# Kernel tuning notes

Hardware: AMD Instinct MI355X
Metric: run time of the kernel (lower is better)

The kernel has to match this reference:

```python
import jax, jax.numpy as jnp
import numpy as np
from jax import lax
from itertools import product

KS = 3          # kernel_size
PAD = 1         # padding
N = KS ** 3     # 27 sample points per voxel


def _conv3d_3x3(x, w, b):
    # x: [b,c,D,H,W], w: [O,c,3,3,3]
    out = lax.conv_general_dilated(x, w, (1, 1, 1), [(PAD, PAD)] * 3,
                                   dimension_numbers=('NCDHW', 'OIDHW', 'NCDHW'))
    return out + b[None, :, None, None, None]


def setup_inputs() -> dict:
    key = jax.random.key(0)
    k1, k2, k3, k4 = jax.random.split(key, 4)
    B, C, D, OUTC = 2, 32, 24, 64
    x = jax.random.normal(k1, (B, C, D, D, D), jnp.float32)
    p_w = jax.random.normal(k2, (3 * N, C, KS, KS, KS), jnp.float32) * 0.02
    p_b = jax.random.normal(k3, (3 * N,), jnp.float32) * 0.02
    conv_w = jax.random.normal(k4, (OUTC, C * N), jnp.float32) / np.sqrt(C * N)
    return {"x": x, "p_w": p_w, "p_b": p_b, "conv_w": conv_w}


def reference(x, p_w, p_b, conv_w):
    b, c, h, w, d = x.shape
    # offset prediction: [b, 3N, h, w, d]
    offset = _conv3d_3x3(x, p_w, p_b)

    # p_n: kernel-relative offsets, p_0: base grid (shifted by +1 for padding)
    r = np.arange(-(KS - 1) // 2, (KS - 1) // 2 + 1)
    gx, gy, gz = np.meshgrid(r, r, r, indexing='ij')
    p_n = jnp.asarray(np.concatenate([gx.ravel(), gy.ravel(), gz.ravel()])
                      .reshape(1, 3 * N, 1, 1, 1), jnp.float32)
    ox, oy, oz = np.meshgrid(np.arange(1, h + 1), np.arange(1, w + 1),
                             np.arange(1, d + 1), indexing='ij')
    def rep(a):
        return np.broadcast_to(a.reshape(1, 1, h, w, d), (1, N, h, w, d))
    p_0 = jnp.asarray(np.concatenate([rep(ox), rep(oy), rep(oz)], axis=1), jnp.float32)

    p = p_0 + p_n + offset                      # [b, 3N, h, w, d]
    p = jnp.transpose(p, (0, 2, 3, 4, 1))        # [b, h, w, d, 3N]

    xp = jnp.pad(x, ((0, 0), (0, 0), (PAD, PAD), (PAD, PAD), (PAD, PAD)))
    sizes = (xp.shape[2], xp.shape[3], xp.shape[4])
    ps = [p[..., :N], p[..., N:2 * N], p[..., 2 * N:]]

    qs, ql, pm = [], [], []
    for ax in range(3):
        s = sizes[ax]
        f = jnp.floor(ps[ax])
        qs.append(jnp.clip(f, 0, s - 1).astype(jnp.int32))
        ql.append(jnp.clip(f + 1, 0, s - 1).astype(jnp.int32))
        # out-of-range mask: snap p to its floor (matches torch detach + floor_p)
        m = lax.stop_gradient(((ps[ax] < PAD) | (ps[ax] > s - 1 - PAD)).astype(ps[ax].dtype))
        pa = ps[ax] * (1 - m) + f * m
        pm.append(jnp.clip(pa, 0, s - 1))

    def gather(xb, qi, qj, qk):
        return xb[:, qi, qj, qk]  # [c, h, w, d, N]

    acc = jnp.zeros((b, c, h, w, d, N), x.dtype)
    for cx, cy, cz in product((0, 1), repeat=3):   # 8 trilinear corners
        bits = (cx, cy, cz)
        q = [qs[a] if bits[a] == 0 else ql[a] for a in range(3)]
        g = jnp.ones_like(pm[0])
        for a in range(3):
            diff = q[a].astype(pm[a].dtype) - pm[a]
            g = g * ((1 + diff) if bits[a] == 0 else (1 - diff))
        xq = jax.vmap(gather)(xp, q[0], q[1], q[2])  # [b, c, h, w, d, N]
        acc = acc + g[:, None] * xq

    # [b,c,h,w,d,N] -> [b, c*N, h, w, d] (c-major, N-minor, as in torch view)
    x_off = jnp.transpose(acc, (0, 1, 5, 2, 3, 4)).reshape(b, c * N, h, w, d)
    out = jnp.einsum('oi,bidhw->bodhw', conv_w, x_off)
    p_out = jnp.concatenate(pm, axis=-1)
    return out, p_out
```

## Files before the change

kernel.cpp:

```cpp
#include <hip/hip_runtime.h>

#define CC 32
#define DIM 24
#define SP (DIM*DIM*DIM)
#define NPTS 27
#define M3 81
#define OUTC 64
#define BATCH 2
#define CN (CC*NPTS)

#define VBB 12
#define NV (NPTS*VBB)
#define CPAD 896
#define MP 84
#define HROW 26
#define HALOF (32*3*4*HROW)

typedef __attribute__((ext_vector_type(8))) short short8;
typedef __attribute__((ext_vector_type(4))) float f32x4;

__device__ __forceinline__ unsigned short f2bf(float f) {
    unsigned u = __builtin_bit_cast(unsigned, f);
    return (unsigned short)((u + 0x7FFFu + ((u >> 16) & 1u)) >> 16);
}

__global__ __launch_bounds__(256)
void prep_w_kernel(const float* __restrict__ p_w,
                   const float* __restrict__ conv_w,
                   float* __restrict__ p_wTP,
                   unsigned short* __restrict__ conv_wbf) {
    int id = blockIdx.x * 256 + threadIdx.x;
    if (id < CN * MP) {
        int k = id / MP, m = id % MP;
        p_wTP[id] = (m < M3) ? p_w[(size_t)m * CN + k] : 0.f;
    }
    if (id < CN * OUTC) {
        int o = id / CN, kp = id % CN;
        int n = kp >> 5, c = kp & 31;
        conv_wbf[id] = f2bf(conv_w[(size_t)o * CN + c * NPTS + n]);
    }
}

__global__ __launch_bounds__(256)
void transpose_x_kernel(const float* __restrict__ x,
                        unsigned short* __restrict__ x_t) {
    __shared__ float tile[CC][65];
    int b = blockIdx.x / 216;
    int sp0 = (blockIdx.x % 216) * 64;
    const float* xb = x + (size_t)b * CC * SP;
    for (int it = threadIdx.x; it < CC * 64; it += 256) {
        int c = it >> 6, s = it & 63;
        tile[c][s] = xb[(size_t)c * SP + sp0 + s];
    }
    __syncthreads();
    unsigned short* xtb = x_t + (size_t)b * SP * CC;
    for (int it = threadIdx.x; it < CC * 64; it += 256) {
        int s = it >> 5, c = it & 31;
        xtb[(size_t)(sp0 + s) * CC + c] = f2bf(tile[c][s]);
    }
}

__global__ __launch_bounds__(512, 4)
void offset_gemm_kernel(const float* __restrict__ x,
                        const float* __restrict__ p_wTP,
                        const float* __restrict__ p_b,
                        float* __restrict__ offset) {
    __shared__ float lds[HALOF];

    int bid = blockIdx.x;
    int jp = bid % 12;
    int i  = (bid / 12) % 24;
    int b  = bid / 288;
    int j0 = jp * 2;
    int sp0 = i * 576 + j0 * 24;
    int t = threadIdx.x;

    for (int it = t; it < HALOF; it += 512) {
        int rh = it / HROW, u = it - rh * HROW;
        int c = rh / 12, r2 = rh - c * 12;
        int di = r2 >> 2, jq = r2 & 3;
        int ii = i + di - 1, jj = j0 - 1 + jq, kk = u - 1;
        bool v = ((unsigned)ii < (unsigned)DIM) && ((unsigned)jj < (unsigned)DIM) &&
                 ((unsigned)kk < (unsigned)DIM);
        lds[it] =
            v ? x[((size_t)(b * CC + c) * SP) + ii * 576 + jj * 24 + kk] : 0.f;
    }
    __syncthreads();

    int w = t >> 6, l = t & 63;
    int mt = l / 3, vt = l % 3;
    bool act = (l < 63);
    if (mt > 20) mt = 20;

    float acc[4][8], ac2[4][8];
    #pragma unroll
    for (int a = 0; a < 4; ++a)
        #pragma unroll
        for (int e = 0; e < 8; ++e) { acc[a][e] = 0.f; ac2[a][e] = 0.f; }

    const float* gw = p_wTP + (size_t)(w * 108) * MP + mt * 4;

    for (int cdij = 0; cdij < 36; ++cdij) {
        int c = 4 * w + cdij / 9;
        int dij = cdij % 9;
        int di = dij / 3, dj = dij % 3;
        const float* xrA = lds + ((c * 3 + di) * 4 + dj) * HROW + vt * 8;
        const float* xrB = xrA + HROW;

        float2 a0 = *(const float2*)(xrA);
        float2 a1 = *(const float2*)(xrA + 2);
        float2 a2 = *(const float2*)(xrA + 4);
        float2 a3 = *(const float2*)(xrA + 6);
        float2 a4 = *(const float2*)(xrA + 8);
        float xvA[10] = { a0.x, a0.y, a1.x, a1.y, a2.x, a2.y,
                          a3.x, a3.y, a4.x, a4.y };
        float2 b0 = *(const float2*)(xrB);
        float2 b1 = *(const float2*)(xrB + 2);
        float2 b2 = *(const float2*)(xrB + 4);
        float2 b3 = *(const float2*)(xrB + 6);
        float2 b4 = *(const float2*)(xrB + 8);
        float xvB[10] = { b0.x, b0.y, b1.x, b1.y, b2.x, b2.y,
                          b3.x, b3.y, b4.x, b4.y };

        const float* wr = gw + (size_t)(cdij * 3) * MP;
        #pragma unroll
        for (int dk = 0; dk < 3; ++dk) {
            float4 wv = *(const float4*)(wr + (size_t)dk * MP);
            #pragma unroll
            for (int e = 0; e < 8; ++e) {
                float xa = xvA[dk + e];
                float xb = xvB[dk + e];
                acc[0][e] += wv.x * xa;  ac2[0][e] += wv.x * xb;
                acc[1][e] += wv.y * xa;  ac2[1][e] += wv.y * xb;
                acc[2][e] += wv.z * xa;  ac2[2][e] += wv.z * xb;
                acc[3][e] += wv.w * xa;  ac2[3][e] += wv.w * xb;
            }
        }
    }
    __syncthreads();

    float* part = lds;
    #define STORE_P(W)                                                      \
        do {                                                                \
            float* dst = &part[((W) * MP + mt * 4) * 48 + vt * 8];          \
            _Pragma("unroll")                                               \
            for (int a = 0; a < 4; ++a) {                                   \
                _Pragma("unroll")                                           \
                for (int e2 = 0; e2 < 2; ++e2) {                            \
                    *(float4*)&dst[a * 48 + e2 * 4] =                       \
                        make_float4(acc[a][e2*4], acc[a][e2*4+1],           \
                                    acc[a][e2*4+2], acc[a][e2*4+3]);        \
                    *(float4*)&dst[a * 48 + 24 + e2 * 4] =                  \
                        make_float4(ac2[a][e2*4], ac2[a][e2*4+1],           \
                                    ac2[a][e2*4+2], ac2[a][e2*4+3]);        \
                }                                                           \
            }                                                               \
        } while (0)
    #define ADD_P(W)                                                       \
        do {                                                                \
            float* dst = &part[((W) * MP + mt * 4) * 48 + vt * 8];          \
            _Pragma("unroll")                                               \
            for (int a = 0; a < 4; ++a) {                                   \
                _Pragma("unroll")                                           \
                for (int e2 = 0; e2 < 2; ++e2) {                            \
                    float4 p = *(const float4*)&dst[a * 48 + e2 * 4];       \
                    p.x += acc[a][e2*4];   p.y += acc[a][e2*4+1];           \
                    p.z += acc[a][e2*4+2]; p.w += acc[a][e2*4+3];           \
                    *(float4*)&dst[a * 48 + e2 * 4] = p;                    \
                    float4 q = *(const float4*)&dst[a * 48 + 24 + e2 * 4];  \
                    q.x += ac2[a][e2*4];   q.y += ac2[a][e2*4+1];           \
                    q.z += ac2[a][e2*4+2]; q.w += ac2[a][e2*4+3];           \
                    *(float4*)&dst[a * 48 + 24 + e2 * 4] = q;               \
                }                                                           \
            }                                                               \
        } while (0)

    if (act && w < 2) STORE_P(w);
    __syncthreads();
    if (act && (w == 2 || w == 3)) ADD_P(w - 2);
    __syncthreads();
    if (act && (w == 4 || w == 5)) ADD_P(w - 4);
    __syncthreads();
    if (act && (w == 6 || w == 7)) ADD_P(w - 6);
    __syncthreads();
    #undef STORE_P
    #undef ADD_P

    for (int it = t; it < M3 * 12; it += 512) {
        int m = it / 12, vq = it % 12;
        float4 p0 = *(const float4*)&part[(m) * 48 + vq * 4];
        float4 p1 = *(const float4*)&part[(MP + m) * 48 + vq * 4];
        float bias = p_b[m];
        float4 s = make_float4(p0.x + p1.x + bias, p0.y + p1.y + bias,
                               p0.z + p1.z + bias, p0.w + p1.w + bias);
        *(float4*)&offset[((size_t)(b * M3 + m)) * SP + sp0 + vq * 4] = s;
    }
}

__global__ __launch_bounds__(256, 4)
void sample_gemm_kernel(const unsigned short* __restrict__ x_t,
                        const float* __restrict__ offset,
                        const unsigned short* __restrict__ conv_wbf,
                        float* __restrict__ out,
                        float* __restrict__ p_out) {
    __shared__ __align__(16) unsigned char region[VBB * CPAD * 2 + 8 * NV * 4];
    unsigned short* col = (unsigned short*)region;
    unsigned* s_corner = (unsigned*)(region + VBB * CPAD * 2);

    int bid = blockIdx.x;
    int r = bid & 1;
    int j = (bid >> 1) % 24;
    int i = ((bid >> 1) / 24) % 24;
    int b = bid / 1152;
    int k0 = r * VBB;
    int sp0 = i * 576 + j * 24 + k0;
    int t = threadIdx.x;

    const unsigned short* xtb = x_t + (size_t)b * SP * CC;

    for (int it = t; it < NV; it += 256) {
        int v = it % VBB, n = it / VBB;
        int sp = sp0 + v;
        int k = k0 + v;

        int pnx = n / 9 - 1, pny = (n / 3) % 3 - 1, pnz = n % 3 - 1;
        float p0a[3] = { (float)(i + 1 + pnx),
                         (float)(j + 1 + pny),
                         (float)(k + 1 + pnz) };
        int ql[3], qh[3];
        float wl[3], wh[3];
        #pragma unroll
        for (int ax = 0; ax < 3; ++ax) {
            int m = ax * NPTS + n;
            float p = p0a[ax] + offset[((size_t)(b * M3 + m)) * SP + sp];
            float f = floorf(p);
            int qlo = (int)fminf(fmaxf(f,       0.f), 25.f);
            int qhi = (int)fminf(fmaxf(f + 1.f, 0.f), 25.f);
            bool oob = (p < 1.f) || (p > 24.f);
            float pa = oob ? f : p;
            float pm = fminf(fmaxf(pa, 0.f), 25.f);
            ql[ax] = qlo; qh[ax] = qhi;
            wl[ax] = 1.f + ((float)qlo - pm);
            wh[ax] = 1.f - ((float)qhi - pm);
            p_out[((size_t)(b * SP + sp)) * M3 + m] = pm;
        }

        #pragma unroll
        for (int cr = 0; cr < 8; ++cr) {
            int ii = ((cr & 4) ? qh[0] : ql[0]) - 1;
            int jj = ((cr & 2) ? qh[1] : ql[1]) - 1;
            int kk = ((cr & 1) ? qh[2] : ql[2]) - 1;
            bool valid = ((unsigned)ii < (unsigned)DIM) &&
                         ((unsigned)jj < (unsigned)DIM) &&
                         ((unsigned)kk < (unsigned)DIM);
            float cw = ((cr & 4) ? wh[0] : wl[0]) *
                       ((cr & 2) ? wh[1] : wl[1]) *
                       ((cr & 1) ? wh[2] : wl[2]);
            unsigned idx = (unsigned)(ii * 576 + jj * 24 + kk);
            s_corner[cr * NV + it] =
                valid ? ((idx << 16) | (unsigned)f2bf(cw)) : 0u;
        }
    }
    __syncthreads();

    for (int task = t; task < NV * 4; task += 256) {
        int item = task >> 2, q = task & 3;
        int v = item % VBB, n = item / VBB;

        const unsigned short* xq = xtb + q * 8;
        float acc[8];
        #pragma unroll
        for (int e = 0; e < 8; ++e) acc[e] = 0.f;

        #pragma unroll
        for (int cr = 0; cr < 8; ++cr) {
            unsigned u = s_corner[cr * NV + item];
            float wc = __builtin_bit_cast(float, u << 16);
            const unsigned* s = (const unsigned*)(xq + (size_t)(u >> 16) * CC);
            #pragma unroll
            for (int q2 = 0; q2 < 4; ++q2) {
                unsigned uu = s[q2];
                acc[2 * q2]     += wc * __builtin_bit_cast(float, uu << 16);
                acc[2 * q2 + 1] += wc * __builtin_bit_cast(float, uu & 0xFFFF0000u);
            }
        }

        short8 pk;
        #pragma unroll
        for (int e = 0; e < 8; ++e)
            pk[e] = (short)f2bf(acc[e]);
        int sv = (v & 7) << 3;
        *(short8*)&col[v * CPAD + ((n * 32 + q * 8) ^ sv)] = pk;
    }
    __syncthreads();

    {
        int mt = t >> 6;
        int l = t & 63;
        int lr = l & 15;
        int g = l >> 4;
        int sv = (lr & 7) << 3;

        const short8* ap =
            (const short8*)(conv_wbf + ((size_t)(mt * 16 + lr)) * CN + g * 8);
        const unsigned short* bp = col + lr * CPAD;

        f32x4 acc = {0.f, 0.f, 0.f, 0.f};
        #pragma unroll 3
        for (int kb = 0; kb < CN / 32; ++kb) {
            short8 a = ap[kb * 4];
            short8 bb = *(const short8*)&bp[(kb * 32 + g * 8) ^ sv];
            acc = __builtin_amdgcn_mfma_f32_16x16x32_bf16(a, bb, acc, 0, 0, 0);
        }
        if (lr < VBB) {
            float* op = out + ((size_t)(b * OUTC + mt * 16 + g * 4)) * SP + sp0 + lr;
            #pragma unroll
            for (int rr = 0; rr < 4; ++rr)
                op[(size_t)rr * SP] = acc[rr];
        }
    }
}

extern "C" void kernel_launch(void* const* d_in, const int* in_sizes, int n_in,
                              void* d_out, int out_size, void* d_ws, size_t ws_size,
                              hipStream_t stream) {
    const float* x      = (const float*)d_in[0];
    const float* p_w    = (const float*)d_in[1];
    const float* p_b    = (const float*)d_in[2];
    const float* conv_w = (const float*)d_in[3];

    float* out_all = (float*)d_out;
    float* out_main = out_all;
    float* p_out    = out_all + (size_t)BATCH * OUTC * SP;

    float* offset          = (float*)d_ws;
    float* p_wTP           = offset + (size_t)BATCH * M3 * SP;
    unsigned short* conv_wbf = (unsigned short*)(p_wTP + (size_t)CN * MP);
    unsigned short* x_t    = conv_wbf + (size_t)CN * OUTC;

    {
        int total = CN * MP;
        prep_w_kernel<<<(total + 255) / 256, 256, 0, stream>>>(p_w, conv_w,
                                                               p_wTP, conv_wbf);
    }
    {
        int blocks = BATCH * (SP / 64);
        transpose_x_kernel<<<blocks, 256, 0, stream>>>(x, x_t);
    }
    {
        int blocks = BATCH * 24 * 12;
        offset_gemm_kernel<<<blocks, 512, 0, stream>>>(x, p_wTP, p_b, offset);
    }
    {
        int blocks = BATCH * 24 * 24 * 2;
        sample_gemm_kernel<<<blocks, 256, 0, stream>>>(x_t, offset, conv_wbf,
                                                       out_main, p_out);
    }
}
```

Baseline: 123.5 us.

## Restructure offset conv: wave-per-output-channel-slice with scalar weights, drop LDS reduction

```diff
diff --git a/kernel.cpp b/kernel.cpp
--- a/kernel.cpp
+++ b/kernel.cpp
@@ -14,7 +14,7 @@
 #define CPAD 896
 #define MP 84
 #define HROW 26
-#define HALOF (32*3*4*HROW)
+#define HALOF (CC*3*4*HROW)
 
 typedef __attribute__((ext_vector_type(8))) short short8;
 typedef __attribute__((ext_vector_type(4))) float f32x4;
@@ -60,12 +60,12 @@
     }
 }
 
-__global__ __launch_bounds__(512, 4)
+__global__ __launch_bounds__(256, 4)
 void offset_gemm_kernel(const float* __restrict__ x,
                         const float* __restrict__ p_wTP,
                         const float* __restrict__ p_b,
                         float* __restrict__ offset) {
-    __shared__ float lds[HALOF];
+    __shared__ float halo[HALOF];
 
     int bid = blockIdx.x;
     int jp = bid % 12;
@@ -75,125 +75,57 @@
     int sp0 = i * 576 + j0 * 24;
     int t = threadIdx.x;
 
-    for (int it = t; it < HALOF; it += 512) {
+    for (int it = t; it < HALOF; it += 256) {
         int rh = it / HROW, u = it - rh * HROW;
         int c = rh / 12, r2 = rh - c * 12;
         int di = r2 >> 2, jq = r2 & 3;
         int ii = i + di - 1, jj = j0 - 1 + jq, kk = u - 1;
         bool v = ((unsigned)ii < (unsigned)DIM) && ((unsigned)jj < (unsigned)DIM) &&
                  ((unsigned)kk < (unsigned)DIM);
-        lds[it] =
+        halo[it] =
             v ? x[((size_t)(b * CC + c) * SP) + ii * 576 + jj * 24 + kk] : 0.f;
     }
     __syncthreads();
 
-    int w = t >> 6, l = t & 63;
-    int mt = l / 3, vt = l % 3;
-    bool act = (l < 63);
-    if (mt > 20) mt = 20;
-
-    float acc[4][8], ac2[4][8];
+    int l = t & 63;
+    int wu = __builtin_amdgcn_readfirstlane(t >> 6);
+    bool act = (l < 48);
+    int vl = act ? l : 47;
+    int jrow = vl / 24, kv = vl - jrow * 24;
+    int lane_base = jrow * HROW + kv;
+
+    float acc[21];
     #pragma unroll
-    for (int a = 0; a < 4; ++a)
-        #pragma unroll
-        for (int e = 0; e < 8; ++e) { acc[a][e] = 0.f; ac2[a][e] = 0.f; }
-
-    const float* gw = p_wTP + (size_t)(w * 108) * MP + mt * 4;
-
-    for (int cdij = 0; cdij < 36; ++cdij) {
-        int c = 4 * w + cdij / 9;
-        int dij = cdij % 9;
-        int di = dij / 3, dj = dij % 3;
-        const float* xrA = lds + ((c * 3 + di) * 4 + dj) * HROW + vt * 8;
-        const float* xrB = xrA + HROW;
-
-        float2 a0 = *(const float2*)(xrA);
-        float2 a1 = *(const float2*)(xrA + 2);
-        float2 a2 = *(const float2*)(xrA + 4);
-        float2 a3 = *(const float2*)(xrA + 6);
-        float2 a4 = *(const float2*)(xrA + 8);
-        float xvA[10] = { a0.x, a0.y, a1.x, a1.y, a2.x, a2.y,
-                          a3.x, a3.y, a4.x, a4.y };
-        float2 b0 = *(const float2*)(xrB);
-        float2 b1 = *(const float2*)(xrB + 2);
-        float2 b2 = *(const float2*)(xrB + 4);
-        float2 b3 = *(const float2*)(xrB + 6);
-        float2 b4 = *(const float2*)(xrB + 8);
-        float xvB[10] = { b0.x, b0.y, b1.x, b1.y, b2.x, b2.y,
-                          b3.x, b3.y, b4.x, b4.y };
-
-        const float* wr = gw + (size_t)(cdij * 3) * MP;
-        #pragma unroll
-        for (int dk = 0; dk < 3; ++dk) {
-            float4 wv = *(const float4*)(wr + (size_t)dk * MP);
+    for (int mm = 0; mm < 21; ++mm) acc[mm] = 0.f;
+
+    const float* wbase = p_wTP + 21 * wu;
+
+    for (int c = 0; c < CC; ++c) {
+        const float* hb = halo + c * (3 * 4 * HROW) + lane_base;
+        const float* wc = wbase + (size_t)(c * 27) * MP;
+        #pragma unroll
+        for (int dij = 0; dij < 9; ++dij) {
+            int di = dij / 3, dj = dij % 3;
+            const float* hrow = hb + (di * 4 + dj) * HROW;
             #pragma unroll
-            for (int e = 0; e < 8; ++e) {
-                float xa = xvA[dk + e];
-                float xb = xvB[dk + e];
-                acc[0][e] += wv.x * xa;  ac2[0][e] += wv.x * xb;
-                acc[1][e] += wv.y * xa;  ac2[1][e] += wv.y * xb;
-                acc[2][e] += wv.z * xa;  ac2[2][e] += wv.z * xb;
-                acc[3][e] += wv.w * xa;  ac2[3][e] += wv.w * xb;
+            for (int dk = 0; dk < 3; ++dk) {
+                float xv = hrow[dk];
+                const float* wr = wc + (size_t)(dij * 3 + dk) * MP;
+                #pragma unroll
+                for (int mm = 0; mm < 21; ++mm)
+                    acc[mm] += wr[mm] * xv;
             }
         }
     }
-    __syncthreads();
-
-    float* part = lds;
-    #define STORE_P(W)                                                      \
-        do {                                                                \
-            float* dst = &part[((W) * MP + mt * 4) * 48 + vt * 8];          \
-            _Pragma("unroll")                                               \
-            for (int a = 0; a < 4; ++a) {                                   \
-                _Pragma("unroll")                                           \
-                for (int e2 = 0; e2 < 2; ++e2) {                            \
-                    *(float4*)&dst[a * 48 + e2 * 4] =                       \
-                        make_float4(acc[a][e2*4], acc[a][e2*4+1],           \
-                                    acc[a][e2*4+2], acc[a][e2*4+3]);        \
-                    *(float4*)&dst[a * 48 + 24 + e2 * 4] =                  \
-                        make_float4(ac2[a][e2*4], ac2[a][e2*4+1],           \
-                                    ac2[a][e2*4+2], ac2[a][e2*4+3]);        \
-                }                                                           \
-            }                                                               \
-        } while (0)
-    #define ADD_P(W)                                                       \
-        do {                                                                \
-            float* dst = &part[((W) * MP + mt * 4) * 48 + vt * 8];          \
-            _Pragma("unroll")                                               \
-            for (int a = 0; a < 4; ++a) {                                   \
-                _Pragma("unroll")                                           \
-                for (int e2 = 0; e2 < 2; ++e2) {                            \
-                    float4 p = *(const float4*)&dst[a * 48 + e2 * 4];       \
-                    p.x += acc[a][e2*4];   p.y += acc[a][e2*4+1];           \
-                    p.z += acc[a][e2*4+2]; p.w += acc[a][e2*4+3];           \
-                    *(float4*)&dst[a * 48 + e2 * 4] = p;                    \
-                    float4 q = *(const float4*)&dst[a * 48 + 24 + e2 * 4];  \
-                    q.x += ac2[a][e2*4];   q.y += ac2[a][e2*4+1];           \
-                    q.z += ac2[a][e2*4+2]; q.w += ac2[a][e2*4+3];           \
-                    *(float4*)&dst[a * 48 + 24 + e2 * 4] = q;               \
-                }                                                           \
-            }                                                               \
-        } while (0)
-
-    if (act && w < 2) STORE_P(w);
-    __syncthreads();
-    if (act && (w == 2 || w == 3)) ADD_P(w - 2);
-    __syncthreads();
-    if (act && (w == 4 || w == 5)) ADD_P(w - 4);
-    __syncthreads();
-    if (act && (w == 6 || w == 7)) ADD_P(w - 6);
-    __syncthreads();
-    #undef STORE_P
-    #undef ADD_P
-
-    for (int it = t; it < M3 * 12; it += 512) {
-        int m = it / 12, vq = it % 12;
-        float4 p0 = *(const float4*)&part[(m) * 48 + vq * 4];
-        float4 p1 = *(const float4*)&part[(MP + m) * 48 + vq * 4];
-        float bias = p_b[m];
-        float4 s = make_float4(p0.x + p1.x + bias, p0.y + p1.y + bias,
-                               p0.z + p1.z + bias, p0.w + p1.w + bias);
-        *(float4*)&offset[((size_t)(b * M3 + m)) * SP + sp0 + vq * 4] = s;
+
+    if (act) {
+        int spv = sp0 + jrow * 24 + kv;
+        #pragma unroll
+        for (int mm = 0; mm < 21; ++mm) {
+            int m = 21 * wu + mm;
+            if (m < M3)
+                offset[((size_t)(b * M3 + m)) * SP + spv] = acc[mm] + p_b[m];
+        }
     }
 }
 
@@ -349,7 +281,7 @@
     }
     {
         int blocks = BATCH * 24 * 12;
-        offset_gemm_kernel<<<blocks, 512, 0, stream>>>(x, p_wTP, p_b, offset);
+        offset_gemm_kernel<<<blocks, 256, 0, stream>>>(x, p_wTP, p_b, offset);
     }
     {
         int blocks = BATCH * 24 * 24 * 2;
```

Result: slower. 179.1 us (+45.1%).
